# Performance work log

Hardware: AMD Instinct MI355X
Metric: run time of the kernel (lower is better)

Reference implementation:

```python
import jax, jax.numpy as jnp
import numpy as np

B, S, D, H, FF = 4, 1024, 1024, 16, 4096
DH = D // H
EPS = 1e-5


def setup_inputs() -> dict:
    key = jax.random.key(0)
    ks = jax.random.split(key, 24)
    w = lambda i, shp: jax.random.normal(ks[i], shp, jnp.float32) * 0.02
    inp = {
        'tgt': jax.random.normal(ks[0], (B, S, D), jnp.float32),
        'memory': jax.random.normal(ks[1], (B, S, D), jnp.float32),
        'mask': jax.random.randint(ks[2], (B, S, S), 0, 2, jnp.int32),
        # self-attention projections (stored [in,out]; torch Linear weight transposed)
        'sa_wq': w(3, (D, D)), 'sa_bq': jnp.zeros((D,), jnp.float32),
        'sa_wk': w(4, (D, D)), 'sa_bk': jnp.zeros((D,), jnp.float32),
        'sa_wv': w(5, (D, D)), 'sa_bv': jnp.zeros((D,), jnp.float32),
        'sa_wo': w(6, (D, D)), 'sa_bo': jnp.zeros((D,), jnp.float32),
        # cross-attention projections
        'ca_wq': w(7, (D, D)), 'ca_bq': jnp.zeros((D,), jnp.float32),
        'ca_wk': w(8, (D, D)), 'ca_bk': jnp.zeros((D,), jnp.float32),
        'ca_wv': w(9, (D, D)), 'ca_bv': jnp.zeros((D,), jnp.float32),
        'ca_wo': w(10, (D, D)), 'ca_bo': jnp.zeros((D,), jnp.float32),
        # FFN
        'w1': w(11, (D, FF)), 'b1': jnp.zeros((FF,), jnp.float32),
        'w2': w(12, (FF, D)), 'b2': jnp.zeros((D,), jnp.float32),
        # LayerNorms
        'g1': jnp.ones((D,), jnp.float32), 'be1': jnp.zeros((D,), jnp.float32),
        'g2': jnp.ones((D,), jnp.float32), 'be2': jnp.zeros((D,), jnp.float32),
        'g3': jnp.ones((D,), jnp.float32), 'be3': jnp.zeros((D,), jnp.float32),
    }
    return inp


def _layernorm(x, g, b):
    m = jnp.mean(x, axis=-1, keepdims=True)
    v = jnp.mean((x - m) ** 2, axis=-1, keepdims=True)
    return (x - m) * jax.lax.rsqrt(v + EPS) * g + b


def _mha(x, y, mask, wq, bq, wk, bk, wv, bv, wo, bo):
    # chunk(h,-1)+cat(0) head-split == reshape to [B,S,H,DH]
    b_, sq, _ = x.shape
    sk = y.shape[1]
    q = (x @ wq + bq).reshape(b_, sq, H, DH)
    k = (y @ wk + bk).reshape(b_, sk, H, DH)
    v = (y @ wv + bv).reshape(b_, sk, H, DH)
    score = jnp.einsum('bqhd,bkhd->bhqk', q, k) / jnp.float32(np.sqrt(DH))
    score = score + (1.0 - mask[:, None].astype(score.dtype)) * (-1e9)
    attn = jax.nn.softmax(score, axis=-1)
    out = jnp.einsum('bhqk,bkhd->bqhd', attn, v).reshape(b_, sq, D)
    return out @ wo + bo


def reference(tgt, memory, mask,
              sa_wq, sa_bq, sa_wk, sa_bk, sa_wv, sa_bv, sa_wo, sa_bo,
              ca_wq, ca_bq, ca_wk, ca_bk, ca_wv, ca_bv, ca_wo, ca_bo,
              w1, b1, w2, b2, g1, be1, g2, be2, g3, be3):
    t = tgt + _mha(tgt, tgt, mask, sa_wq, sa_bq, sa_wk, sa_bk, sa_wv, sa_bv, sa_wo, sa_bo)
    t = _layernorm(t, g1, be1)
    t = t + _mha(t, memory, mask, ca_wq, ca_bq, ca_wk, ca_bk, ca_wv, ca_bv, ca_wo, ca_bo)
    t = _layernorm(t, g2, be2)
    t = t + (jax.nn.relu(t @ w1 + b1) @ w2 + b2)
    t = _layernorm(t, g3, be3)
    return t
```

## Files before the change

### kernel.cpp

```cpp
#include <hip/hip_runtime.h>
#include <math.h>

typedef float f32x4 __attribute__((ext_vector_type(4)));
typedef unsigned short ushort8 __attribute__((ext_vector_type(8)));
typedef unsigned short ushort4v __attribute__((ext_vector_type(4)));
typedef __bf16 bf16x8 __attribute__((ext_vector_type(8)));
typedef unsigned int u32;

__device__ __forceinline__ unsigned short f2bf(float x) {
  union { float f; unsigned u; } v; v.f = x;
  unsigned r = v.u + 0x7FFFu + ((v.u >> 16) & 1u);
  return (unsigned short)(r >> 16);
}
__device__ __forceinline__ float bf2f(unsigned short u) {
  union { unsigned u; float f; } c; c.u = ((unsigned)u) << 16; return c.f;
}

__device__ __forceinline__ f32x4 mfma16(ushort8 a, ushort8 b, f32x4 c) {
  return __builtin_amdgcn_mfma_f32_16x16x32_bf16(
      __builtin_bit_cast(bf16x8, a), __builtin_bit_cast(bf16x8, b), c, 0, 0, 0);
}

__device__ __forceinline__ void gload16(const void* g, void* l) {
  __builtin_amdgcn_global_load_lds((const __attribute__((address_space(1))) u32*)g,
                                   (__attribute__((address_space(3))) u32*)l, 16, 0, 0);
}

__device__ __forceinline__ int xcd_swz(int orig, int nwg) {
  int q = nwg >> 3, r = nwg & 7;
  int xcd = orig & 7, lid = orig >> 3;
  return (xcd < r ? xcd * (q + 1) : r * (q + 1) + (xcd - r) * q) + lid;
}

__global__ __launch_bounds__(256) void gemm_bf16_kernel(
    const unsigned short* __restrict__ A, const unsigned short* __restrict__ A2,
    int nsplit, const unsigned short* __restrict__ Bt,
    const float* __restrict__ bias, void* __restrict__ C,
    int M, int N, int K, int flags)
{
  __shared__ __align__(16) char As0[128 * 128];
  __shared__ __align__(16) char Bs0[128 * 128];
  __shared__ __align__(16) char As1[128 * 128];
  __shared__ __align__(16) char Bs1[128 * 128];
  const int gx = gridDim.x;
  const int wg = xcd_swz(blockIdx.x + gx * blockIdx.y, gx * gridDim.y);
  const int bn = wg % gx, bm = wg / gx;
  const int z = blockIdx.z;
  const int t = threadIdx.x;
  const int lane = t & 63, w = t >> 6, wm = w >> 1, wn = w & 1;
  const int l4 = lane & 15, lg = lane >> 4;
  const size_t K2 = (size_t)K * 2;

  f32x4 acc[4][4];
#pragma unroll
  for (int i = 0; i < 4; ++i)
#pragma unroll
    for (int j = 0; j < 4; ++j) acc[i][j] = f32x4{0.f, 0.f, 0.f, 0.f};

  const int lr = lane >> 3;
  const int ls = (lane & 7) ^ lr;
  const unsigned short* Ause = (bn < nsplit) ? A : A2;
  const char* Ag = (const char*)Ause + (size_t)(bm * 128 + w * 32 + lr) * K2 + ls * 16;
  const char* Bg = (const char*)Bt + (size_t)(bn * 128 + w * 32 + lr) * K2 + ls * 16;
  const int wo = w * 4096;

  auto STAGE = [&](char* Al, char* Bl, int kt) {
    const size_t ko = (size_t)kt * 128;
#pragma unroll
    for (int i = 0; i < 4; ++i) {
      gload16(Ag + i * 8 * K2 + ko, Al + wo + i * 1024);
      gload16(Bg + i * 8 * K2 + ko, Bl + wo + i * 1024);
    }
  };
  auto COMPUTE = [&](const char* As, const char* Bs) {
#pragma unroll
    for (int ks = 0; ks < 2; ++ks) {
      const int kb = ks * 64 + lg * 16;
      ushort8 af[4], bfr[4];
#pragma unroll
      for (int mi = 0; mi < 4; ++mi) {
        int r = wm * 64 + mi * 16 + l4;
        af[mi] = *reinterpret_cast<const ushort8*>(As + r * 128 + (kb ^ ((r & 7) << 4)));
      }
#pragma unroll
      for (int ni = 0; ni < 4; ++ni) {
        int r = wn * 64 + ni * 16 + l4;
        bfr[ni] = *reinterpret_cast<const ushort8*>(Bs + r * 128 + (kb ^ ((r & 7) << 4)));
      }
#pragma unroll
      for (int mi = 0; mi < 4; ++mi)
#pragma unroll
        for (int ni = 0; ni < 4; ++ni)
          acc[mi][ni] = mfma16(af[mi], bfr[ni], acc[mi][ni]);
    }
  };

#define GWAIT(more) do { if (more) asm volatile("s_waitcnt vmcnt(8)" ::: "memory"); \
                         else      asm volatile("s_waitcnt vmcnt(0)" ::: "memory"); } while (0)

  const int nkt2 = (K >> 6) / gridDim.z;
  const int kbeg = z * nkt2, kend = kbeg + nkt2;
  STAGE(As0, Bs0, kbeg);
  STAGE(As1, Bs1, kbeg + 1);
  for (int kt = kbeg; kt < kend; kt += 2) {
    GWAIT(kt + 1 < kend);
    __builtin_amdgcn_s_barrier();
    __builtin_amdgcn_sched_barrier(0);
    COMPUTE(As0, Bs0);
    __builtin_amdgcn_s_barrier();
    __builtin_amdgcn_sched_barrier(0);
    if (kt + 2 < kend) STAGE(As0, Bs0, kt + 2);
    GWAIT(kt + 2 < kend);
    __builtin_amdgcn_s_barrier();
    __builtin_amdgcn_sched_barrier(0);
    COMPUTE(As1, Bs1);
    __builtin_amdgcn_s_barrier();
    __builtin_amdgcn_sched_barrier(0);
    if (kt + 3 < kend) STAGE(As1, Bs1, kt + 3);
  }
#undef GWAIT

  const int relu = flags & 1, obf = flags & 2;
#pragma unroll
  for (int mi = 0; mi < 4; ++mi)
#pragma unroll
    for (int ni = 0; ni < 4; ++ni) {
      int col = bn * 128 + wn * 64 + ni * 16 + l4;
      float bia = (z == 0) ? bias[col] : 0.f;
#pragma unroll
      for (int j = 0; j < 4; ++j) {
        int row = bm * 128 + wm * 64 + mi * 16 + lg * 4 + j;
        float vv = acc[mi][ni][j] + bia;
        if (relu) vv = fmaxf(vv, 0.f);
        size_t idx = (size_t)z * M * N + (size_t)row * N + col;
        if (obf) ((unsigned short*)C)[idx] = f2bf(vv);
        else     ((float*)C)[idx] = vv;
      }
    }
}

constexpr int kS = 1024, kD = 1024, kDH = 64;

__global__ __launch_bounds__(512) void attn_kernel(
    const unsigned short* __restrict__ Qg, const unsigned short* __restrict__ Kg,
    const unsigned short* __restrict__ Vg, int qs, int ks_,
    const unsigned short* __restrict__ mpack, unsigned short* __restrict__ Og)
{
  __shared__ __align__(16) char Ks0[8192];
  __shared__ __align__(16) char Ks1[8192];
  __shared__ __align__(16) char VT0[8192];
  __shared__ __align__(16) char VT1[8192];
  __shared__ __align__(16) char Ps[16384];
  const int wg = xcd_swz(blockIdx.x + 8 * (blockIdx.y + 16 * blockIdx.z), 512);
  const int qt = wg & 7, h = (wg >> 3) & 15, b = wg >> 7;
  const int t = threadIdx.x, lane = t & 63, w = t >> 6;
  const int l4 = lane & 15, lg = lane >> 4;
  const int lr = lane >> 3, sg = (lane & 7) ^ lr;

  ushort8 q0, q1;
  {
    const unsigned short* src = Qg + (size_t)(b * kS + qt * 128 + w * 16 + l4) * qs + h * kDH;
    q0 = *reinterpret_cast<const ushort8*>(src + lg * 8);
    q1 = *reinterpret_cast<const ushort8*>(src + 32 + lg * 8);
  }
  ushort8 onesv;
#pragma unroll
  for (int i = 0; i < 8; ++i) onesv[i] = 0x3F80;

  const unsigned short* mtb = mpack + (size_t)(b * 8 + qt) * 8192 + t;

  auto stageK = [&](char* Kl, int kt) {
    const char* base = (const char*)(Kg + (size_t)(b * kS + kt * 64) * ks_ + h * kDH) + sg * 16;
    gload16(base + (size_t)(w * 8 + lr) * (ks_ * 2), Kl + w * 1024);
  };

  float m_r[4];
  f32x4 l_acc = f32x4{0.f, 0.f, 0.f, 0.f};
  f32x4 o[4];
#pragma unroll
  for (int j = 0; j < 4; ++j) m_r[j] = -1e30f;
#pragma unroll
  for (int di = 0; di < 4; ++di) o[di] = f32x4{0.f, 0.f, 0.f, 0.f};

  ushort8 vA, vB;
  unsigned short mA, mB;
  stageK(Ks0, 0);
  {
    const unsigned short* vsrc = Vg + (size_t)(b * kS + (t >> 3)) * ks_ + h * kDH + (t & 7) * 8;
    vA = *reinterpret_cast<const ushort8*>(vsrc);
    mA = mtb[0];
  }

#define ATTN_TILE(KC, VC, KN, VCC, VNN, MCUR, MNXT, KTV)                                 \
  {                                                                                      \
    asm volatile("s_waitcnt vmcnt(0)" ::: "memory");                                     \
    {       \
      int key2 = (t >> 3) * 2, c0 = (t & 7) * 8;                                         \
      _Pragma("unroll")                                                                  \
      for (int i = 0; i < 8; ++i) {                                                      \
        int dh = c0 + i;                                                                 \
        *(unsigned short*)(VC + dh * 128 +                                               \
            (key2 ^ ((dh & 7) << 4) ^ ((dh >> 4) << 5))) = VCC[i];                       \
      }                                                                                  \
    }                                                                                    \
    asm volatile("s_waitcnt lgkmcnt(0)" ::: "memory");                                   \
    __builtin_amdgcn_s_barrier();                                                        \
    __builtin_amdgcn_sched_barrier(0);                                                   \
    if ((KTV) + 1 < 16) {                  \
      stageK(KN, (KTV) + 1);                                                             \
      const unsigned short* vsrc = Vg +                                                  \
          (size_t)(b * kS + ((KTV) + 1) * 64 + (t >> 3)) * ks_ + h * kDH + (t & 7) * 8;  \
      VNN = *reinterpret_cast<const ushort8*>(vsrc);                                     \
      MNXT = mtb[((KTV) + 1) * 512];                                                     \
    }                                                                                    \
    f32x4 sc[4];                                                                         \
    _Pragma("unroll")                                                                    \
    for (int ni = 0; ni < 4; ++ni) sc[ni] = f32x4{0.f, 0.f, 0.f, 0.f};                   \
    __builtin_amdgcn_s_setprio(1);                                                       \
    _Pragma("unroll")                                                                    \
    for (int ks = 0; ks < 2; ++ks) {                                                     \
      const int kb = ks * 64 + lg * 16;                                                  \
      ushort8 a = ks ? q1 : q0;                                                          \
      _Pragma("unroll")                                                                  \
      for (int ni = 0; ni < 4; ++ni) {                                                   \
        int kr = ni * 16 + l4;                                                           \
        ushort8 bb = *(const ushort8*)(KC + kr * 128 + (kb ^ ((kr & 7) << 4)));          \
        sc[ni] = mfma16(a, bb, sc[ni]);                                                  \
      }                                                                                  \
    }                                                                                    \
    __builtin_amdgcn_s_setprio(0);                                                       \
    const unsigned mbits_ = (unsigned)(MCUR);                                            \
    float tmax[4];                                                                       \
    _Pragma("unroll")                                                                    \
    for (int j = 0; j < 4; ++j) {                                                        \
      _Pragma("unroll")                                                                  \
      for (int ni = 0; ni < 4; ++ni)                                                     \
        if (!((mbits_ >> (ni * 4 + j)) & 1u)) sc[ni][j] = -1e9f;                         \
      tmax[j] = fmaxf(fmaxf(sc[0][j], sc[1][j]), fmaxf(sc[2][j], sc[3][j]));             \
    }                                                                                    \
    bool need = (tmax[0] > m_r[0] + 8.f) || (tmax[1] > m_r[1] + 8.f) ||                  \
                (tmax[2] > m_r[2] + 8.f) || (tmax[3] > m_r[3] + 8.f);                    \
    if (__any(need)) {                 \
      _Pragma("unroll")                                                                  \
      for (int j = 0; j < 4; ++j) {                                                      \
        tmax[j] = fmaxf(tmax[j], __shfl_xor(tmax[j], 1, 64));                            \
        tmax[j] = fmaxf(tmax[j], __shfl_xor(tmax[j], 2, 64));                            \
        tmax[j] = fmaxf(tmax[j], __shfl_xor(tmax[j], 4, 64));                            \
        tmax[j] = fmaxf(tmax[j], __shfl_xor(tmax[j], 8, 64));                            \
        float mn = fmaxf(m_r[j], tmax[j]);                                               \
        float al = exp2f(m_r[j] - mn);                                                   \
        m_r[j] = mn;                                                                     \
        o[0][j] *= al; o[1][j] *= al; o[2][j] *= al; o[3][j] *= al;                      \
        l_acc[j] *= al;                                                                  \
      }                                                                                  \
    }                                                                                    \
    _Pragma("unroll")                                                                    \
    for (int ni = 0; ni < 4; ++ni)                                                       \
      _Pragma("unroll")                                                                  \
      for (int j = 0; j < 4; ++j)                                                        \
        sc[ni][j] = exp2f(sc[ni][j] - m_r[j]);                                           \
    {                               \
      char* Pw = Ps + w * 2048;                                                          \
      _Pragma("unroll")                                                                  \
      for (int ni = 0; ni < 4; ++ni)                                                     \
        _Pragma("unroll")                                                                \
        for (int j = 0; j < 4; ++j) {                                                    \
          int row = lg * 4 + j, col = ni * 16 + l4;                                      \
          *(unsigned short*)(Pw + row * 128 +                                            \
              ((col * 2) ^ ((row & 7) << 4) ^ ((row & 8) << 2))) =                       \
              __builtin_bit_cast(unsigned short, (__bf16)sc[ni][j]);                     \
        }                                                                                \
    }                                                                                    \
    asm volatile("s_waitcnt lgkmcnt(0)" ::: "memory");                                   \
    __builtin_amdgcn_sched_barrier(0);                                                   \
    __builtin_amdgcn_s_setprio(1);                                                       \
    {                                             \
      const char* Pw = Ps + w * 2048;                                                    \
      _Pragma("unroll")                                                                  \
      for (int ks = 0; ks < 2; ++ks) {                                                   \
        const int kb = ks * 64 + lg * 16;                                                \
        ushort8 pa = *(const ushort8*)(Pw + l4 * 128 +                                   \
            (kb ^ ((l4 & 7) << 4) ^ ((l4 & 8) << 2)));                                   \
        l_acc = mfma16(pa, onesv, l_acc);                                                \
        _Pragma("unroll")                                                                \
        for (int di = 0; di < 4; ++di) {                                                 \
          int vr2 = di * 16 + l4;                                                        \
          ushort8 vb = *(const ushort8*)(VC + vr2 * 128 +                                \
              (kb ^ ((vr2 & 7) << 4) ^ ((vr2 >> 4) << 5)));                              \
          o[di] = mfma16(pa, vb, o[di]);                                                 \
        }                                                                                \
      }                                                                                  \
    }                                                                                    \
    __builtin_amdgcn_s_setprio(0);                                                       \
  }

  for (int kt = 0; kt < 16; kt += 2) {
    ATTN_TILE(Ks0, VT0, Ks1, vA, vB, mA, mB, kt);
    ATTN_TILE(Ks1, VT1, Ks0, vB, vA, mB, mA, kt + 1);
  }
#undef ATTN_TILE

  float rinv[4];
#pragma unroll
  for (int j = 0; j < 4; ++j) rinv[j] = 1.0f / l_acc[j];
#pragma unroll
  for (int di = 0; di < 4; ++di) {
    int col = h * kDH + di * 16 + l4;
#pragma unroll
    for (int j = 0; j < 4; ++j) {
      int qrow = qt * 128 + w * 16 + lg * 4 + j;
      Og[(size_t)(b * kS + qrow) * kD + col] =
          __builtin_bit_cast(unsigned short, (__bf16)(o[di][j] * rinv[j]));
    }
  }
}

__global__ __launch_bounds__(256) void addln_kernel(
    const unsigned short* __restrict__ x, const unsigned short* __restrict__ y0,
    const unsigned short* __restrict__ y1,
    const float* __restrict__ g, const float* __restrict__ be,
    unsigned short* __restrict__ outb, float* __restrict__ outf)
{
  const int row = blockIdx.x, t = threadIdx.x;
  const size_t base = (size_t)row * 1024 + t * 4;
  ushort4v xv = *reinterpret_cast<const ushort4v*>(x + base);
  ushort4v yv0 = *reinterpret_cast<const ushort4v*>(y0 + base);
  ushort4v yv1 = *reinterpret_cast<const ushort4v*>(y1 + base);
  float v0 = bf2f(xv[0]) + bf2f(yv0[0]) + bf2f(yv1[0]);
  float v1 = bf2f(xv[1]) + bf2f(yv0[1]) + bf2f(yv1[1]);
  float v2 = bf2f(xv[2]) + bf2f(yv0[2]) + bf2f(yv1[2]);
  float v3 = bf2f(xv[3]) + bf2f(yv0[3]) + bf2f(yv1[3]);
  float s1 = v0 + v1 + v2 + v3;
  float s2 = v0 * v0 + v1 * v1 + v2 * v2 + v3 * v3;
#pragma unroll
  for (int off = 1; off < 64; off <<= 1) {
    s1 += __shfl_xor(s1, off, 64);
    s2 += __shfl_xor(s2, off, 64);
  }
  __shared__ float r1[4], r2[4];
  const int w = t >> 6, lane = t & 63;
  if (lane == 0) { r1[w] = s1; r2[w] = s2; }
  __syncthreads();
  s1 = r1[0] + r1[1] + r1[2] + r1[3];
  s2 = r2[0] + r2[1] + r2[2] + r2[3];
  const float mean = s1 * (1.0f / 1024.0f);
  const float var = s2 * (1.0f / 1024.0f) - mean * mean;
  const float rs = rsqrtf(var + 1e-5f);
  float4 gv = *reinterpret_cast<const float4*>(g + t * 4);
  float4 bv = *reinterpret_cast<const float4*>(be + t * 4);
  float4 ov;
  ov.x = (v0 - mean) * rs * gv.x + bv.x;
  ov.y = (v1 - mean) * rs * gv.y + bv.y;
  ov.z = (v2 - mean) * rs * gv.z + bv.z;
  ov.w = (v3 - mean) * rs * gv.w + bv.w;
  if (outb) {
    ushort4v bo;
    bo[0] = f2bf(ov.x); bo[1] = f2bf(ov.y); bo[2] = f2bf(ov.z); bo[3] = f2bf(ov.w);
    *reinterpret_cast<ushort4v*>(outb + base) = bo;
  }
  if (outf) *reinterpret_cast<float4*>(outf + base) = ov;
}

__global__ __launch_bounds__(256) void cvt2_bf16_kernel(
    const float* __restrict__ a, const float* __restrict__ b,
    unsigned short* __restrict__ da, unsigned short* __restrict__ db, int n8each)
{
  int i = blockIdx.x * 256 + threadIdx.x;
  const float* s = a; unsigned short* d = da;
  if (i >= n8each) { s = b; d = db; i -= n8each; }
  if (i >= n8each) return;
  float4 f0 = reinterpret_cast<const float4*>(s)[i * 2];
  float4 f1 = reinterpret_cast<const float4*>(s)[i * 2 + 1];
  ushort8 v;
  v[0] = f2bf(f0.x); v[1] = f2bf(f0.y); v[2] = f2bf(f0.z); v[3] = f2bf(f0.w);
  v[4] = f2bf(f1.x); v[5] = f2bf(f1.y); v[6] = f2bf(f1.z); v[7] = f2bf(f1.w);
  reinterpret_cast<ushort8*>(d)[i] = v;
}

__global__ __launch_bounds__(256) void transpose_cvt_kernel(
    const float* __restrict__ src, unsigned short* __restrict__ dst, int K, int N)
{
  __shared__ float tile[32][33];
  const int bx = blockIdx.x, by = blockIdx.y;
  const int tx = threadIdx.x & 31, ty = threadIdx.x >> 5;
#pragma unroll
  for (int i = 0; i < 4; ++i)
    tile[ty + i * 8][tx] = src[(size_t)(by * 32 + ty + i * 8) * N + bx * 32 + tx];
  __syncthreads();
#pragma unroll
  for (int i = 0; i < 4; ++i)
    dst[(size_t)(bx * 32 + ty + i * 8) * K + by * 32 + tx] = f2bf(tile[tx][ty + i * 8]);
}

struct TPtrs { const float* s[8]; unsigned short* d[8]; float scale[8]; };
__global__ __launch_bounds__(256) void tcvt_batch_kernel(TPtrs p)
{
  __shared__ float tile[32][33];
  const float* __restrict__ src = p.s[blockIdx.z];
  unsigned short* __restrict__ dst = p.d[blockIdx.z];
  const float sc = p.scale[blockIdx.z];
  const int bx = blockIdx.x, by = blockIdx.y;
  const int tx = threadIdx.x & 31, ty = threadIdx.x >> 5;
#pragma unroll
  for (int i = 0; i < 4; ++i)
    tile[ty + i * 8][tx] = src[(size_t)(by * 32 + ty + i * 8) * 1024 + bx * 32 + tx];
  __syncthreads();
#pragma unroll
  for (int i = 0; i < 4; ++i)
    dst[(size_t)(bx * 32 + ty + i * 8) * 1024 + by * 32 + tx] = f2bf(tile[tx][ty + i * 8] * sc);
}

__global__ void biasprep_kernel(const float* sq, const float* sk, const float* sv,
                                const float* cq, const float* ck, const float* cv,
                                float* bsa, float* bca, float s)
{
  int i = blockIdx.x * 256 + threadIdx.x;
  if (i < 1024)      { bsa[i] = sq[i] * s;        bca[i] = cq[i] * s; }
  else if (i < 2048) { bsa[i] = sk[i - 1024];     bca[i] = ck[i - 1024]; }
  else if (i < 3072) { bsa[i] = sv[i - 2048];     bca[i] = cv[i - 2048]; }
}

__global__ __launch_bounds__(256) void maskprep_kernel(
    const int* __restrict__ mask, unsigned short* __restrict__ mpack)
{
  int idx = blockIdx.x * 256 + threadIdx.x;
  int t = idx & 511;
  int kt = (idx >> 9) & 15;
  int qt = (idx >> 13) & 7;
  int b = idx >> 16;
  int qb = qt * 128 + ((t >> 6) & 7) * 16 + ((t >> 4) & 3) * 4;
  int kb = kt * 64 + (t & 15);
  unsigned m = 0;
#pragma unroll
  for (int ni = 0; ni < 4; ++ni)
#pragma unroll
    for (int j = 0; j < 4; ++j)
      if (mask[(size_t)(b * 1024 + qb + j) * 1024 + kb + ni * 16]) m |= 1u << (ni * 4 + j);
  mpack[idx] = (unsigned short)m;
}

extern "C" void kernel_launch(void* const* d_in, const int* in_sizes, int n_in,
                              void* d_out, int out_size, void* d_ws, size_t ws_size,
                              hipStream_t stream)
{
  const float* tgt  = (const float*)d_in[0];
  const float* memi = (const float*)d_in[1];
  const int*   mask = (const int*)d_in[2];
  const float* sa_wq = (const float*)d_in[3];  const float* sa_bq = (const float*)d_in[4];
  const float* sa_wk = (const float*)d_in[5];  const float* sa_bk = (const float*)d_in[6];
  const float* sa_wv = (const float*)d_in[7];  const float* sa_bv = (const float*)d_in[8];
  const float* sa_wo = (const float*)d_in[9];  const float* sa_bo = (const float*)d_in[10];
  const float* ca_wq = (const float*)d_in[11]; const float* ca_bq = (const float*)d_in[12];
  const float* ca_wk = (const float*)d_in[13]; const float* ca_bk = (const float*)d_in[14];
  const float* ca_wv = (const float*)d_in[15]; const float* ca_bv = (const float*)d_in[16];
  const float* ca_wo = (const float*)d_in[17]; const float* ca_bo = (const float*)d_in[18];
  const float* w1 = (const float*)d_in[19]; const float* b1 = (const float*)d_in[20];
  const float* w2 = (const float*)d_in[21]; const float* b2 = (const float*)d_in[22];
  const float* g1 = (const float*)d_in[23]; const float* be1 = (const float*)d_in[24];
  const float* g2 = (const float*)d_in[25]; const float* be2 = (const float*)d_in[26];
  const float* g3 = (const float*)d_in[27]; const float* be3 = (const float*)d_in[28];
  float* out = (float*)d_out;
  char* W = (char*)d_ws;
  const size_t MB = 1 << 20;
  typedef unsigned short us;
  const float QSCALE = 0.18033688011112042f;

  us* Wsaqkv = (us*)(W + 0);
  us* Wsao   = (us*)(W + 6 * MB);
  us* Wcaqkv = (us*)(W + 8 * MB);
  us* Wcao   = (us*)(W + 14 * MB);
  us* W1t    = (us*)(W + 16 * MB);
  us* W2t    = (us*)(W + 24 * MB);
  float* b_saqkv = (float*)(W + 32 * MB);
  float* b_caqkv = (float*)(W + 32 * MB + 16384);
  us* tgt_bf = (us*)(W + 33 * MB);
  us* T2b    = tgt_bf;
  us* mem_bf = (us*)(W + 41 * MB);
  us* QKV    = (us*)(W + 49 * MB);
  us* AO     = (us*)(W + 73 * MB);
  us* Hb     = (us*)(W + 49 * MB);
  us* Opb    = (us*)(W + 81 * MB);
  us* mpack  = (us*)(W + 97 * MB);
  us* T1b    = (us*)(W + 98 * MB);
  us* Opb1   = Opb + 4096 * 1024;

  const int M = 4096;
  dim3 blk(256);
  auto gemm = [&](const us* Aa, const us* Aa2, int nsplit, const us* Bta,
                  const float* bias, void* Cc, int Nn, int Kk, int flags, int zsplit) {
    gemm_bf16_kernel<<<dim3(Nn / 128, M / 128, zsplit), blk, 0, stream>>>(
        Aa, Aa2, nsplit, Bta, bias, Cc, M, Nn, Kk, flags);
  };

  TPtrs tp;
  tp.s[0] = sa_wq; tp.d[0] = Wsaqkv;               tp.scale[0] = QSCALE;
  tp.s[1] = sa_wk; tp.d[1] = Wsaqkv + 1024 * 1024; tp.scale[1] = 1.f;
  tp.s[2] = sa_wv; tp.d[2] = Wsaqkv + 2048 * 1024; tp.scale[2] = 1.f;
  tp.s[3] = sa_wo; tp.d[3] = Wsao;                 tp.scale[3] = 1.f;
  tp.s[4] = ca_wq; tp.d[4] = Wcaqkv;               tp.scale[4] = QSCALE;
  tp.s[5] = ca_wk; tp.d[5] = Wcaqkv + 1024 * 1024; tp.scale[5] = 1.f;
  tp.s[6] = ca_wv; tp.d[6] = Wcaqkv + 2048 * 1024; tp.scale[6] = 1.f;
  tp.s[7] = ca_wo; tp.d[7] = Wcao;                 tp.scale[7] = 1.f;
  tcvt_batch_kernel<<<dim3(32, 32, 8), blk, 0, stream>>>(tp);
  transpose_cvt_kernel<<<dim3(128, 32), blk, 0, stream>>>(w1, W1t, 1024, 4096);
  transpose_cvt_kernel<<<dim3(32, 128), blk, 0, stream>>>(w2, W2t, 4096, 1024);
  cvt2_bf16_kernel<<<dim3(4096), blk, 0, stream>>>(tgt, memi, tgt_bf, mem_bf, M * 1024 / 8);
  biasprep_kernel<<<dim3(12), blk, 0, stream>>>(sa_bq, sa_bk, sa_bv, ca_bq, ca_bk, ca_bv,
                                                b_saqkv, b_caqkv, QSCALE);
  maskprep_kernel<<<dim3(1024), blk, 0, stream>>>(mask, mpack);

  gemm(tgt_bf, tgt_bf, 1 << 30, Wsaqkv, b_saqkv, QKV, 3072, 1024, 2, 1);
  attn_kernel<<<dim3(8, 16, 4), dim3(512), 0, stream>>>(QKV, QKV + 1024, QKV + 2048, 3072, 3072, mpack, AO);
  gemm(AO, AO, 1 << 30, Wsao, sa_bo, Opb, 1024, 1024, 2, 2);
  addln_kernel<<<dim3(M), blk, 0, stream>>>(tgt_bf, Opb, Opb1, g1, be1, T1b, nullptr);

  gemm(T1b, mem_bf, 8, Wcaqkv, b_caqkv, QKV, 3072, 1024, 2, 1);
  attn_kernel<<<dim3(8, 16, 4), dim3(512), 0, stream>>>(QKV, QKV + 1024, QKV + 2048, 3072, 3072, mpack, AO);
  gemm(AO, AO, 1 << 30, Wcao, ca_bo, Opb, 1024, 1024, 2, 2);
  addln_kernel<<<dim3(M), blk, 0, stream>>>(T1b, Opb, Opb1, g2, be2, T2b, nullptr);

  gemm(T2b, T2b, 1 << 30, W1t, b1, Hb, 4096, 1024, 3, 1);
  gemm(Hb, Hb, 1 << 30, W2t, b2, Opb, 1024, 4096, 2, 2);
  addln_kernel<<<dim3(M), blk, 0, stream>>>(T2b, Opb, Opb1, g3, be3, nullptr, out);

  (void)in_sizes; (void)n_in; (void)out_size; (void)ws_size;
}
```

Baseline: 378.4 us.

## Process 128-key tiles per attention iteration with a single transposed-V buffer

The attention kernel now handles 128 keys per loop iteration instead of 64, halving the iteration count and the per-iteration barrier and softmax-rescale overhead. K is still double-buffered, with two async loads per thread. V is now staged into one shared transposed buffer after the top barrier, and a second barrier before the PV stage makes sure all waves have finished writing it. LDS use rises to about 80KB per block and more score registers are live, which may lower occupancy and add a barrier stall per iteration.

```diff
diff --git a/kernel.cpp b/kernel.cpp
--- a/kernel.cpp
+++ b/kernel.cpp
@@ -146,11 +146,10 @@
     const unsigned short* __restrict__ Vg, int qs, int ks_,
     const unsigned short* __restrict__ mpack, unsigned short* __restrict__ Og)
 {
-  __shared__ __align__(16) char Ks0[8192];
-  __shared__ __align__(16) char Ks1[8192];
-  __shared__ __align__(16) char VT0[8192];
-  __shared__ __align__(16) char VT1[8192];
-  __shared__ __align__(16) char Ps[16384];
+  __shared__ __align__(16) char Ks0[16384];
+  __shared__ __align__(16) char Ks1[16384];
+  __shared__ __align__(16) char VTs[16384];
+  __shared__ __align__(16) char Ps[32768];
   const int wg = xcd_swz(blockIdx.x + 8 * (blockIdx.y + 16 * blockIdx.z), 512);
   const int qt = wg & 7, h = (wg >> 3) & 15, b = wg >> 7;
   const int t = threadIdx.x, lane = t & 63, w = t >> 6;
@@ -169,9 +168,10 @@
 
   const unsigned short* mtb = mpack + (size_t)(b * 8 + qt) * 8192 + t;
 
-  auto stageK = [&](char* Kl, int kt) {
-    const char* base = (const char*)(Kg + (size_t)(b * kS + kt * 64) * ks_ + h * kDH) + sg * 16;
-    gload16(base + (size_t)(w * 8 + lr) * (ks_ * 2), Kl + w * 1024);
+  auto stageK = [&](char* Kl, int it) {
+    const char* base = (const char*)(Kg + (size_t)(b * kS + it * 128) * ks_ + h * kDH) + sg * 16;
+    gload16(base + (size_t)(w * 16 + lr) * (ks_ * 2), Kl + w * 2048);
+    gload16(base + (size_t)(w * 16 + 8 + lr) * (ks_ * 2), Kl + w * 2048 + 1024);
   };
 
   float m_r[4];
@@ -182,61 +182,75 @@
 #pragma unroll
   for (int di = 0; di < 4; ++di) o[di] = f32x4{0.f, 0.f, 0.f, 0.f};
 
-  ushort8 vA, vB;
-  unsigned short mA, mB;
+  ushort8 vA0, vA1, vB0, vB1;
+  unsigned short mA0, mA1, mB0, mB1;
   stageK(Ks0, 0);
   {
-    const unsigned short* vsrc = Vg + (size_t)(b * kS + (t >> 3)) * ks_ + h * kDH + (t & 7) * 8;
-    vA = *reinterpret_cast<const ushort8*>(vsrc);
-    mA = mtb[0];
-  }
-
-#define ATTN_TILE(KC, VC, KN, VCC, VNN, MCUR, MNXT, KTV)                                 \
+    const unsigned short* vsrc = Vg + (size_t)(b * kS + (t >> 2)) * ks_ + h * kDH + (t & 3) * 16;
+    vA0 = *reinterpret_cast<const ushort8*>(vsrc);
+    vA1 = *reinterpret_cast<const ushort8*>(vsrc + 8);
+    mA0 = mtb[0];
+    mA1 = mtb[512];
+  }
+
+#define ATTN_IT(KC, KN, V0c, V1c, V0n, V1n, M0c, M1c, M0n, M1n, IT)                      \
   {                                                                                      \
     asm volatile("s_waitcnt vmcnt(0)" ::: "memory");                                     \
-    {       \
-      int key2 = (t >> 3) * 2, c0 = (t & 7) * 8;                                         \
+    __builtin_amdgcn_s_barrier();                                          \
+    __builtin_amdgcn_sched_barrier(0);                                                   \
+    if ((IT) + 1 < 8) {               \
+      stageK(KN, (IT) + 1);                                                              \
+      const unsigned short* vsrc = Vg +                                                  \
+          (size_t)(b * kS + ((IT) + 1) * 128 + (t >> 2)) * ks_ + h * kDH + (t & 3) * 16; \
+      V0n = *reinterpret_cast<const ushort8*>(vsrc);                                     \
+      V1n = *reinterpret_cast<const ushort8*>(vsrc + 8);                                 \
+      M0n = mtb[(2 * (IT) + 2) * 512];                                                   \
+      M1n = mtb[(2 * (IT) + 3) * 512];                                                   \
+    }                                                                                    \
+    {                    \
+      int key2 = (t >> 2) * 2, c0 = (t & 3) * 16;                                        \
       _Pragma("unroll")                                                                  \
       for (int i = 0; i < 8; ++i) {                                                      \
         int dh = c0 + i;                                                                 \
-        *(unsigned short*)(VC + dh * 128 +                                               \
-            (key2 ^ ((dh & 7) << 4) ^ ((dh >> 4) << 5))) = VCC[i];                       \
+        *(unsigned short*)(VTs + dh * 256 +                                              \
+            (key2 ^ ((dh & 7) << 4) ^ ((dh >> 4) << 5))) = V0c[i];                       \
       }                                                                                  \
-    }                                                                                    \
-    asm volatile("s_waitcnt lgkmcnt(0)" ::: "memory");                                   \
-    __builtin_amdgcn_s_barrier();                                                        \
-    __builtin_amdgcn_sched_barrier(0);                                                   \
-    if ((KTV) + 1 < 16) {                  \
-      stageK(KN, (KTV) + 1);                                                             \
-      const unsigned short* vsrc = Vg +                                                  \
-          (size_t)(b * kS + ((KTV) + 1) * 64 + (t >> 3)) * ks_ + h * kDH + (t & 7) * 8;  \
-      VNN = *reinterpret_cast<const ushort8*>(vsrc);                                     \
-      MNXT = mtb[((KTV) + 1) * 512];                                                     \
-    }                                                                                    \
-    f32x4 sc[4];                                                                         \
+      _Pragma("unroll")                                                                  \
+      for (int i = 0; i < 8; ++i) {                                                      \
+        int dh = c0 + 8 + i;                                                             \
+        *(unsigned short*)(VTs + dh * 256 +                                              \
+            (key2 ^ ((dh & 7) << 4) ^ ((dh >> 4) << 5))) = V1c[i];                       \
+      }                                                                                  \
+    }                                                                                    \
+    f32x4 sc[8];                                                                         \
     _Pragma("unroll")                                                                    \
-    for (int ni = 0; ni < 4; ++ni) sc[ni] = f32x4{0.f, 0.f, 0.f, 0.f};                   \
+    for (int ni = 0; ni < 8; ++ni) sc[ni] = f32x4{0.f, 0.f, 0.f, 0.f};                   \
     __builtin_amdgcn_s_setprio(1);                                                       \
     _Pragma("unroll")                                                                    \
     for (int ks = 0; ks < 2; ++ks) {                                                     \
       const int kb = ks * 64 + lg * 16;                                                  \
       ushort8 a = ks ? q1 : q0;                                                          \
       _Pragma("unroll")                                                                  \
-      for (int ni = 0; ni < 4; ++ni) {                                                   \
+      for (int ni = 0; ni < 8; ++ni) {                                                   \
         int kr = ni * 16 + l4;                                                           \
         ushort8 bb = *(const ushort8*)(KC + kr * 128 + (kb ^ ((kr & 7) << 4)));          \
         sc[ni] = mfma16(a, bb, sc[ni]);                                                  \
       }                                                                                  \
     }                                                                                    \
     __builtin_amdgcn_s_setprio(0);                                                       \
-    const unsigned mbits_ = (unsigned)(MCUR);                                            \
+    const unsigned mb0_ = (unsigned)(M0c), mb1_ = (unsigned)(M1c);                       \
     float tmax[4];                                                                       \
     _Pragma("unroll")                                                                    \
     for (int j = 0; j < 4; ++j) {                                                        \
       _Pragma("unroll")                                                                  \
       for (int ni = 0; ni < 4; ++ni)                                                     \
-        if (!((mbits_ >> (ni * 4 + j)) & 1u)) sc[ni][j] = -1e9f;                         \
-      tmax[j] = fmaxf(fmaxf(sc[0][j], sc[1][j]), fmaxf(sc[2][j], sc[3][j]));             \
+        if (!((mb0_ >> (ni * 4 + j)) & 1u)) sc[ni][j] = -1e9f;                           \
+      _Pragma("unroll")                                                                  \
+      for (int ni = 4; ni < 8; ++ni)                                                     \
+        if (!((mb1_ >> ((ni - 4) * 4 + j)) & 1u)) sc[ni][j] = -1e9f;                     \
+      float t0 = fmaxf(fmaxf(sc[0][j], sc[1][j]), fmaxf(sc[2][j], sc[3][j]));            \
+      float t1 = fmaxf(fmaxf(sc[4][j], sc[5][j]), fmaxf(sc[6][j], sc[7][j]));            \
+      tmax[j] = fmaxf(t0, t1);                                                           \
     }                                                                                    \
     bool need = (tmax[0] > m_r[0] + 8.f) || (tmax[1] > m_r[1] + 8.f) ||                  \
                 (tmax[2] > m_r[2] + 8.f) || (tmax[3] > m_r[3] + 8.f);                    \
@@ -255,37 +269,38 @@
       }                                                                                  \
     }                                                                                    \
     _Pragma("unroll")                                                                    \
-    for (int ni = 0; ni < 4; ++ni)                                                       \
+    for (int ni = 0; ni < 8; ++ni)                                                       \
       _Pragma("unroll")                                                                  \
       for (int j = 0; j < 4; ++j)                                                        \
         sc[ni][j] = exp2f(sc[ni][j] - m_r[j]);                                           \
-    {                               \
-      char* Pw = Ps + w * 2048;                                                          \
-      _Pragma("unroll")                                                                  \
-      for (int ni = 0; ni < 4; ++ni)                                                     \
+    {                    \
+      char* Pw = Ps + w * 4096;                                                          \
+      _Pragma("unroll")                                                                  \
+      for (int ni = 0; ni < 8; ++ni)                                                     \
         _Pragma("unroll")                                                                \
         for (int j = 0; j < 4; ++j) {                                                    \
           int row = lg * 4 + j, col = ni * 16 + l4;                                      \
-          *(unsigned short*)(Pw + row * 128 +                                            \
+          *(unsigned short*)(Pw + row * 256 +                                            \
               ((col * 2) ^ ((row & 7) << 4) ^ ((row & 8) << 2))) =                       \
               __builtin_bit_cast(unsigned short, (__bf16)sc[ni][j]);                     \
         }                                                                                \
     }                                                                                    \
     asm volatile("s_waitcnt lgkmcnt(0)" ::: "memory");                                   \
+    __builtin_amdgcn_s_barrier();                                          \
     __builtin_amdgcn_sched_barrier(0);                                                   \
     __builtin_amdgcn_s_setprio(1);                                                       \
-    {                                             \
-      const char* Pw = Ps + w * 2048;                                                    \
-      _Pragma("unroll")                                                                  \
-      for (int ks = 0; ks < 2; ++ks) {                                                   \
+    {                      \
+      const char* Pw = Ps + w * 4096;                                                    \
+      _Pragma("unroll")                                                                  \
+      for (int ks = 0; ks < 4; ++ks) {                                                   \
         const int kb = ks * 64 + lg * 16;                                                \
-        ushort8 pa = *(const ushort8*)(Pw + l4 * 128 +                                   \
+        ushort8 pa = *(const ushort8*)(Pw + l4 * 256 +                                   \
             (kb ^ ((l4 & 7) << 4) ^ ((l4 & 8) << 2)));                                   \
         l_acc = mfma16(pa, onesv, l_acc);                                                \
         _Pragma("unroll")                                                                \
         for (int di = 0; di < 4; ++di) {                                                 \
           int vr2 = di * 16 + l4;                                                        \
-          ushort8 vb = *(const ushort8*)(VC + vr2 * 128 +                                \
+          ushort8 vb = *(const ushort8*)(VTs + vr2 * 256 +                               \
               (kb ^ ((vr2 & 7) << 4) ^ ((vr2 >> 4) << 5)));                              \
           o[di] = mfma16(pa, vb, o[di]);                                                 \
         }                                                                                \
@@ -294,11 +309,11 @@
     __builtin_amdgcn_s_setprio(0);                                                       \
   }
 
-  for (int kt = 0; kt < 16; kt += 2) {
-    ATTN_TILE(Ks0, VT0, Ks1, vA, vB, mA, mB, kt);
-    ATTN_TILE(Ks1, VT1, Ks0, vB, vA, mB, mA, kt + 1);
-  }
-#undef ATTN_TILE
+  for (int it = 0; it < 8; it += 2) {
+    ATTN_IT(Ks0, Ks1, vA0, vA1, vB0, vB1, mA0, mA1, mB0, mB1, it);
+    ATTN_IT(Ks1, Ks0, vB0, vB1, vA0, vA1, mB0, mB1, mA0, mA1, it + 1);
+  }
+#undef ATTN_IT
 
   float rinv[4];
 #pragma unroll
```

After: 384.6 us. About the same (+1.6%).
